# Kernel tuning notes

Hardware: AMD Instinct MI355X
Metric: run time of the kernel (lower is better)

Reference implementation:

```python
import jax, jax.numpy as jnp
import numpy as np

EPS = 1e-06
B, S, H = 4, 4096, 4096


def setup_inputs() -> dict:
    key = jax.random.key(0)
    k1, k2 = jax.random.split(key)
    hidden_states = jax.random.normal(k1, (B, S, H), dtype=jnp.float16)
    # weight near 1.0 like a trained RMSNorm gain
    weight = (1.0 + 0.1 * jax.random.normal(k2, (H,))).astype(jnp.float16)
    return {"hidden_states": hidden_states, "weight": weight}


def reference(hidden_states, weight):
    """RMSNorm (fp32 accumulation) + dynamic per-token int8 quantization.

    Returns (quantized int8 tensor [B,S,H], per-token scale [B,S,1]) matching
    lmdeploy's rms_norm_dynamic_quant -> QTensor(tensor, scale).
    """
    x = hidden_states.astype(jnp.float32)
    var = jnp.mean(x * x, axis=-1, keepdims=True)          # [B,S,1]
    xn = x * jax.lax.rsqrt(var + EPS) * weight.astype(jnp.float32)
    scale = jnp.max(jnp.abs(xn), axis=-1, keepdims=True) / 127.0  # [B,S,1]
    q = jnp.clip(jnp.round(xn / scale), -128.0, 127.0).astype(jnp.int8)
    return q, scale
```

## Files before the change

### kernel.cpp

```cpp
#include <hip/hip_runtime.h>


#define HDIM  4096
#define BLOCK 256
#define PER_T (HDIM / BLOCK)

__global__ __launch_bounds__(BLOCK) void qrms_kernel(
    const float* __restrict__ x,
    const float* __restrict__ w,
    float* __restrict__ qout,
    float* __restrict__ sout)
{
    const int row = blockIdx.x;
    const int t   = threadIdx.x;
    const float* xr = x + (size_t)row * HDIM;

    float p[PER_T];
    float sumsq = 0.0f;
    float amax  = 0.0f;

    #pragma unroll
    for (int c = 0; c < 4; ++c) {
        const int idx = c * (HDIM / 4) + t * 4;
        const float4 xv = *reinterpret_cast<const float4*>(xr + idx);
        const float4 wv = *reinterpret_cast<const float4*>(w  + idx);
        sumsq = fmaf(xv.x, xv.x, sumsq);
        sumsq = fmaf(xv.y, xv.y, sumsq);
        sumsq = fmaf(xv.z, xv.z, sumsq);
        sumsq = fmaf(xv.w, xv.w, sumsq);
        const float p0 = xv.x * wv.x;
        const float p1 = xv.y * wv.y;
        const float p2 = xv.z * wv.z;
        const float p3 = xv.w * wv.w;
        p[c * 4 + 0] = p0;
        p[c * 4 + 1] = p1;
        p[c * 4 + 2] = p2;
        p[c * 4 + 3] = p3;
        amax = fmaxf(amax, fmaxf(fmaxf(fabsf(p0), fabsf(p1)),
                                 fmaxf(fabsf(p2), fabsf(p3))));
    }

    #pragma unroll
    for (int off = 32; off > 0; off >>= 1) {
        sumsq += __shfl_xor(sumsq, off, 64);
        amax   = fmaxf(amax, __shfl_xor(amax, off, 64));
    }

    __shared__ float s_sum[BLOCK / 64];
    __shared__ float s_max[BLOCK / 64];
    const int wave = t >> 6;
    if ((t & 63) == 0) { s_sum[wave] = sumsq; s_max[wave] = amax; }
    __syncthreads();
    const float total = (s_sum[0] + s_sum[1]) + (s_sum[2] + s_sum[3]);
    const float mx    = fmaxf(fmaxf(s_max[0], s_max[1]), fmaxf(s_max[2], s_max[3]));

    const float r      = rsqrtf(total * (1.0f / HDIM) + 1e-6f);
    const float rowmax = mx * r;
    const float qmul   = 127.0f / mx;

    if (t == 0) sout[row] = rowmax * (1.0f / 127.0f);

    float* qr = qout + (size_t)row * HDIM;
    #pragma unroll
    for (int c = 0; c < 4; ++c) {
        const int idx = c * (HDIM / 4) + t * 4;
        float q[4];
        #pragma unroll
        for (int k = 0; k < 4; ++k) {
            float v = rintf(p[c * 4 + k] * qmul);
            q[k] = fminf(127.0f, fmaxf(-128.0f, v));
        }
        *reinterpret_cast<float4*>(qr + idx) = make_float4(q[0], q[1], q[2], q[3]);
    }
}

extern "C" void kernel_launch(void* const* d_in, const int* in_sizes, int n_in,
                              void* d_out, int out_size, void* d_ws, size_t ws_size,
                              hipStream_t stream) {
    const float* x = (const float*)d_in[0];
    const float* w = (const float*)d_in[1];
    float* out = (float*)d_out;
    const int rows = in_sizes[0] / HDIM;
    float* qout = out;
    float* sout = out + (size_t)in_sizes[0];
    qrms_kernel<<<dim3(rows), dim3(BLOCK), 0, stream>>>(x, w, qout, sout);
}
```

Before: 418.9 us.

## Process eight rows per block with hoisted weights and nontemporal stores

```diff
diff --git a/kernel.cpp b/kernel.cpp
--- a/kernel.cpp
+++ b/kernel.cpp
@@ -3,7 +3,9 @@
 
 #define HDIM  4096
 #define BLOCK 256
-#define PER_T (HDIM / BLOCK)
+#define RPB   8
+
+typedef float v4f __attribute__((ext_vector_type(4)));
 
 __global__ __launch_bounds__(BLOCK) void qrms_kernel(
     const float* __restrict__ x,
@@ -11,66 +13,78 @@
     float* __restrict__ qout,
     float* __restrict__ sout)
 {
-    const int row = blockIdx.x;
-    const int t   = threadIdx.x;
-    const float* xr = x + (size_t)row * HDIM;
+    const int t = threadIdx.x;
 
-    float p[PER_T];
-    float sumsq = 0.0f;
-    float amax  = 0.0f;
+    float4 wv[4];
+    #pragma unroll
+    for (int c = 0; c < 4; ++c)
+        wv[c] = *reinterpret_cast<const float4*>(w + c * (HDIM / 4) + t * 4);
 
-    #pragma unroll
-    for (int c = 0; c < 4; ++c) {
-        const int idx = c * (HDIM / 4) + t * 4;
-        const float4 xv = *reinterpret_cast<const float4*>(xr + idx);
-        const float4 wv = *reinterpret_cast<const float4*>(w  + idx);
-        sumsq = fmaf(xv.x, xv.x, sumsq);
-        sumsq = fmaf(xv.y, xv.y, sumsq);
-        sumsq = fmaf(xv.z, xv.z, sumsq);
-        sumsq = fmaf(xv.w, xv.w, sumsq);
-        const float p0 = xv.x * wv.x;
-        const float p1 = xv.y * wv.y;
-        const float p2 = xv.z * wv.z;
-        const float p3 = xv.w * wv.w;
-        p[c * 4 + 0] = p0;
-        p[c * 4 + 1] = p1;
-        p[c * 4 + 2] = p2;
-        p[c * 4 + 3] = p3;
-        amax = fmaxf(amax, fmaxf(fmaxf(fabsf(p0), fabsf(p1)),
-                                 fmaxf(fabsf(p2), fabsf(p3))));
-    }
+    __shared__ float s_sum[2][4];
+    __shared__ float s_max[2][4];
+    const int wave = t >> 6;
 
-    #pragma unroll
-    for (int off = 32; off > 0; off >>= 1) {
-        sumsq += __shfl_xor(sumsq, off, 64);
-        amax   = fmaxf(amax, __shfl_xor(amax, off, 64));
-    }
+    const size_t row0 = (size_t)blockIdx.x * RPB;
+    #pragma unroll 1
+    for (int rr = 0; rr < RPB; ++rr) {
+        const size_t row = row0 + rr;
+        const float* xr = x + row * HDIM;
 
-    __shared__ float s_sum[BLOCK / 64];
-    __shared__ float s_max[BLOCK / 64];
-    const int wave = t >> 6;
-    if ((t & 63) == 0) { s_sum[wave] = sumsq; s_max[wave] = amax; }
-    __syncthreads();
-    const float total = (s_sum[0] + s_sum[1]) + (s_sum[2] + s_sum[3]);
-    const float mx    = fmaxf(fmaxf(s_max[0], s_max[1]), fmaxf(s_max[2], s_max[3]));
+        float p[16];
+        float sumsq = 0.0f;
+        float amax  = 0.0f;
 
-    const float r      = rsqrtf(total * (1.0f / HDIM) + 1e-6f);
-    const float rowmax = mx * r;
-    const float qmul   = 127.0f / mx;
+        #pragma unroll
+        for (int c = 0; c < 4; ++c) {
+            const int idx = c * (HDIM / 4) + t * 4;
+            const float4 xv = *reinterpret_cast<const float4*>(xr + idx);
+            sumsq = fmaf(xv.x, xv.x, sumsq);
+            sumsq = fmaf(xv.y, xv.y, sumsq);
+            sumsq = fmaf(xv.z, xv.z, sumsq);
+            sumsq = fmaf(xv.w, xv.w, sumsq);
+            const float p0 = xv.x * wv[c].x;
+            const float p1 = xv.y * wv[c].y;
+            const float p2 = xv.z * wv[c].z;
+            const float p3 = xv.w * wv[c].w;
+            p[c * 4 + 0] = p0;
+            p[c * 4 + 1] = p1;
+            p[c * 4 + 2] = p2;
+            p[c * 4 + 3] = p3;
+            amax = fmaxf(amax, fmaxf(fmaxf(fabsf(p0), fabsf(p1)),
+                                     fmaxf(fabsf(p2), fabsf(p3))));
+        }
 
-    if (t == 0) sout[row] = rowmax * (1.0f / 127.0f);
+        #pragma unroll
+        for (int off = 32; off > 0; off >>= 1) {
+            sumsq += __shfl_xor(sumsq, off, 64);
+            amax   = fmaxf(amax, __shfl_xor(amax, off, 64));
+        }
 
-    float* qr = qout + (size_t)row * HDIM;
-    #pragma unroll
-    for (int c = 0; c < 4; ++c) {
-        const int idx = c * (HDIM / 4) + t * 4;
-        float q[4];
+        const int b = rr & 1;
+        if ((t & 63) == 0) { s_sum[b][wave] = sumsq; s_max[b][wave] = amax; }
+        __syncthreads();
+        const float total = (s_sum[b][0] + s_sum[b][1]) + (s_sum[b][2] + s_sum[b][3]);
+        const float mx    = fmaxf(fmaxf(s_max[b][0], s_max[b][1]),
+                                  fmaxf(s_max[b][2], s_max[b][3]));
+
+        const float r    = rsqrtf(total * (1.0f / HDIM) + 1e-6f);
+        const float qmul = 127.0f / mx;
+
+        if (t == 0) sout[row] = (mx * r) * (1.0f / 127.0f);
+
+        float* qr = qout + row * HDIM;
         #pragma unroll
-        for (int k = 0; k < 4; ++k) {
-            float v = rintf(p[c * 4 + k] * qmul);
-            q[k] = fminf(127.0f, fmaxf(-128.0f, v));
+        for (int c = 0; c < 4; ++c) {
+            const int idx = c * (HDIM / 4) + t * 4;
+            float q[4];
+            #pragma unroll
+            for (int k = 0; k < 4; ++k) {
+                float v = rintf(p[c * 4 + k] * qmul);
+                q[k] = fminf(127.0f, fmaxf(-128.0f, v));
+            }
+            v4f qv = { q[0], q[1], q[2], q[3] };
+            __builtin_nontemporal_store(qv, reinterpret_cast<v4f*>(qr + idx));
         }
-        *reinterpret_cast<float4*>(qr + idx) = make_float4(q[0], q[1], q[2], q[3]);
     }
 }
 
@@ -83,5 +97,5 @@
     const int rows = in_sizes[0] / HDIM;
     float* qout = out;
     float* sout = out + (size_t)in_sizes[0];
-    qrms_kernel<<<dim3(rows), dim3(BLOCK), 0, stream>>>(x, w, qout, sout);
+    qrms_kernel<<<dim3(rows / RPB), dim3(BLOCK), 0, stream>>>(x, w, qout, sout);
 }
```

After: 455.9 us. 1.09x slower.
